# Kernel optimization log

Measured on AMD Instinct MI355X. Metric: run time of the kernel, lower is better.

Reference implementation:

```python
import jax, jax.numpy as jnp
import numpy as np

C = 1.0          # ball curvature (k = -1/c with c=1.0 in the torch module)
SQC = 1.0        # sqrt(C)
LN_EPS = 1e-5

def _artanh(x):
    return jnp.arctanh(jnp.clip(x, -1.0 + 1e-7, 1.0 - 1e-7))

def _norm(x):
    # last-dim L2 norm, clamped away from zero for stable division
    return jnp.clip(jnp.sqrt(jnp.sum(x * x, axis=-1, keepdims=True)), 1e-7, None)

def expmap0(u):
    un = _norm(u)
    return jnp.tanh(SQC * un) * u / (SQC * un)

def logmap0(y):
    yn = _norm(y)
    return _artanh(SQC * yn) * y / (SQC * yn)

def mobius_add(x, y):
    x2 = jnp.sum(x * x, axis=-1, keepdims=True)
    y2 = jnp.sum(y * y, axis=-1, keepdims=True)
    xy = jnp.sum(x * y, axis=-1, keepdims=True)
    num = (1.0 + 2.0 * C * xy + C * y2) * x + (1.0 - C * x2) * y
    den = 1.0 + 2.0 * C * xy + C * C * x2 * y2
    return num / jnp.clip(den, 1e-15, None)

def mobius_matvec(W, x):
    # W: [H, D], x: [B, D] -> [B, H]
    mx = x @ W.T
    xn = _norm(x)
    mxn = _norm(mx)
    res = jnp.tanh(mxn / xn * _artanh(SQC * xn)) * mx / (SQC * mxn)
    return jnp.where(mxn <= 1e-7, jnp.zeros_like(res), res)

def mobius_pointwise_mul(w, x):
    wx = w * x
    xn = _norm(x)
    wxn = _norm(wx)
    res = jnp.tanh(wxn / xn * _artanh(SQC * xn)) * wx / (SQC * wxn)
    return jnp.where(wxn <= 1e-7, jnp.zeros_like(res), res)

def layer_norm(x, g, b):
    mu = jnp.mean(x, axis=-1, keepdims=True)
    var = jnp.mean((x - mu) ** 2, axis=-1, keepdims=True)
    return (x - mu) * jax.lax.rsqrt(var + LN_EPS) * g + b

def one_rnn_transform(W, h, U, x, b):
    Wh = mobius_matvec(W, h)
    Ux = mobius_matvec(U, x)
    return mobius_add(mobius_add(Wh, Ux), b)

def setup_inputs() -> dict:
    key = jax.random.key(0)
    B, I, H = 65536, 256, 256
    k1, k2, k3, k4, k5 = jax.random.split(key, 5)
    stdv = 1.0 / np.sqrt(H)
    # points on the Poincare ball via expmap0 of small tangent vectors
    x = expmap0(0.02 * jax.random.normal(k1, (B, I), dtype=jnp.float32))
    hx = expmap0(0.02 * jax.random.normal(k2, (B, H), dtype=jnp.float32))
    weight_ih = jax.random.uniform(k3, (3 * H, I), dtype=jnp.float32, minval=-stdv, maxval=stdv)
    weight_hh = jax.random.uniform(k4, (3 * H, H), dtype=jnp.float32, minval=-stdv, maxval=stdv)
    bias = 0.01 * jax.random.normal(k5, (3, H), dtype=jnp.float32)
    ln_gamma = jnp.ones((3, H), dtype=jnp.float32)
    ln_beta = jnp.zeros((3, H), dtype=jnp.float32)
    return {"input": x, "hx": hx, "weight_ih": weight_ih, "weight_hh": weight_hh,
            "bias": bias, "ln_gamma": ln_gamma, "ln_beta": ln_beta}

def reference(input, hx, weight_ih, weight_hh, bias, ln_gamma, ln_beta):
    H = hx.shape[-1]
    W_ir, W_ih_, W_iz = weight_ih[:H], weight_ih[H:2*H], weight_ih[2*H:]
    W_hr, W_hh_, W_hz = weight_hh[:H], weight_hh[H:2*H], weight_hh[2*H:]
    b_r, b_h, b_z = bias[0], bias[1], bias[2]
    temp_z = logmap0(one_rnn_transform(W_hz, hx, W_iz, input, b_z))
    temp_r = logmap0(one_rnn_transform(W_hr, hx, W_ir, input, b_r))
    z_t = jax.nn.sigmoid(layer_norm(temp_z, ln_gamma[0], ln_beta[0]))
    r_t = jax.nn.sigmoid(layer_norm(temp_r, ln_gamma[1], ln_beta[1]))
    rh_t = mobius_pointwise_mul(r_t, hx)
    h_tilde = one_rnn_transform(W_hh_, rh_t, W_ih_, input, b_h)
    h_tilde = expmap0(jnp.tanh(layer_norm(logmap0(h_tilde), ln_gamma[2], ln_beta[2])))
    temp_1 = mobius_pointwise_mul(1.0 - z_t, hx)
    temp_2 = mobius_pointwise_mul(z_t, h_tilde)
    return mobius_add(temp_1, temp_2)
```

## Files before the change

### kernel.cpp

```cpp
#include <hip/hip_runtime.h>
#include <math.h>

#define HD  256
#define BM  16
#define NTH 256

typedef __attribute__((ext_vector_type(8))) short bf16x8;
typedef __attribute__((ext_vector_type(4))) float f32x4;

__device__ __forceinline__ float rcp_f(float x){ return __builtin_amdgcn_rcpf(x); }
__device__ __forceinline__ float tanh_f(float x){
  float ax = fabsf(x);
  float e  = __expf(-2.f*ax);
  float t  = (1.f - e) * rcp_f(1.f + e);
  return copysignf(t, x);
}
__device__ __forceinline__ float artanh_f(float v){
  v = fminf(fmaxf(v, -1.f + 1e-7f), 1.f - 1e-7f);
  return 0.5f * __logf((1.f + v) * rcp_f(1.f - v));
}
__device__ __forceinline__ float sigmoid_f(float v){ return rcp_f(1.f + __expf(-v)); }
__device__ __forceinline__ unsigned short f2bf(float f){
  unsigned u = __float_as_uint(f);
  u += 0x7FFFu + ((u >> 16) & 1u);
  return (unsigned short)(u >> 16);
}
__device__ __forceinline__ float bf2f(unsigned short h){
  return __uint_as_float(((unsigned)h) << 16);
}
__device__ __forceinline__ int swz(int R, int C){
  return R*HD + (((C >> 3) ^ (R & 7)) << 3) + (C & 7);
}

__global__ void convert_w_kernel(const float* __restrict__ Wih,
                                 const float* __restrict__ Whh,
                                 unsigned short* __restrict__ wb){
  int c = blockIdx.x * blockDim.x + threadIdx.x;
  if (c >= 6 * 8192) return;
  int mat = c >> 13;
  int ci  = c & 8191;
  int l = ci & 63, st = ci >> 6;
  int s = st & 7, ct = st >> 3;
  int col = ct * 16 + (l & 15);
  int k0  = s * 32 + (l >> 4) * 8;
  const float* src = (mat < 3) ? (Wih + (size_t)mat * HD * HD)
                               : (Whh + (size_t)(mat - 3) * HD * HD);
  const float* p = src + (size_t)col * HD + k0;
  unsigned short tmp[8];
  #pragma unroll
  for (int j = 0; j < 8; ++j) tmp[j] = f2bf(p[j]);
  *(bf16x8*)(wb + (size_t)mat * 65536 + (size_t)ci * 8) = *(bf16x8*)tmp;
}

__device__ __forceinline__ void gate_gemm(
    const unsigned short* ldsH, const unsigned short* __restrict__ wH,
    const unsigned short* ldsX, const unsigned short* __restrict__ wX,
    f32x4 A[4], f32x4 Bx[4], int wc, int lr, int lg, int l){
  #pragma unroll
  for (int n = 0; n < 4; ++n){
    A[n]  = (f32x4){0.f,0.f,0.f,0.f};
    Bx[n] = (f32x4){0.f,0.f,0.f,0.f};
  }
  #pragma unroll
  for (int s = 0; s < 8; ++s){
    int idx = lr*HD + (((4*s + lg) ^ (lr & 7)) << 3);
    bf16x8 ah = *(const bf16x8*)&ldsH[idx];
    bf16x8 ax = *(const bf16x8*)&ldsX[idx];
    #pragma unroll
    for (int n = 0; n < 4; ++n){
      int ct = wc*4 + n;
      int off = ((ct*8 + s)*64 + l)*8;
      bf16x8 bh = *(const bf16x8*)(wH + off);
      bf16x8 bx = *(const bf16x8*)(wX + off);
      A[n]  = __builtin_amdgcn_mfma_f32_16x16x32_bf16(ah, bh, A[n], 0, 0, 0);
      Bx[n] = __builtin_amdgcn_mfma_f32_16x16x32_bf16(ax, bx, Bx[n], 0, 0, 0);
    }
  }
}

__device__ __forceinline__ void gate_reduce_chain(
    const f32x4 (&A)[4], const f32x4 (&Bx)[4], const float (&bt)[4],
    float (*RED)[33], float (*kco)[9], float (*srow)[BM], const float* sbb,
    int rowA, int gidx, int t, int wc, int lr, int lg){
  float p[7][4];
  #pragma unroll
  for (int q = 0; q < 4; ++q){
    float a2=0.f,b2=0.f,ab=0.f,sA=0.f,sB=0.f,Ab=0.f,Bb=0.f;
    #pragma unroll
    for (int n = 0; n < 4; ++n){
      float ae = A[n][q], be = Bx[n][q], bv = bt[n];
      a2 = fmaf(ae,ae,a2); b2 = fmaf(be,be,b2); ab = fmaf(ae,be,ab);
      sA += ae; sB += be; Ab = fmaf(ae,bv,Ab); Bb = fmaf(be,bv,Bb);
    }
    p[0][q]=a2; p[1][q]=b2; p[2][q]=ab; p[3][q]=sA; p[4][q]=sB; p[5][q]=Ab; p[6][q]=Bb;
  }
  #pragma unroll
  for (int j = 0; j < 7; ++j)
    #pragma unroll
    for (int q = 0; q < 4; ++q){
      float v = p[j][q];
      v += __shfl_xor(v,1); v += __shfl_xor(v,2);
      v += __shfl_xor(v,4); v += __shfl_xor(v,8);
      p[j][q] = v;
    }
  if (lr == 0){
    #pragma unroll
    for (int q = 0; q < 4; ++q){
      int R = lg*4 + q;
      #pragma unroll
      for (int j = 0; j < 7; ++j) RED[R][wc*8 + j] = p[j][q];
    }
  }
  __syncthreads();
  if (t < BM){
    int R = t;
    float s[7];
    #pragma unroll
    for (int j = 0; j < 7; ++j)
      s[j] = RED[R][j] + RED[R][8+j] + RED[R][16+j] + RED[R][24+j];
    float bb  = sbb[gidx];
    float sbs = sbb[4+gidx];
    float an = srow[rowA][R], aa = srow[rowA+1][R];
    float bn = srow[0][R],    ba = srow[1][R];
    float mraw = sqrtf(s[0]); float mA = fmaxf(mraw, 1e-7f);
    float tA = tanh_f(mA / an * aa);
    float sa  = (mraw <= 1e-7f) ? 0.f : tA / mA;
    float x2a = (mraw <= 1e-7f) ? 0.f : tA*tA;
    float nraw = sqrtf(s[1]); float mB = fmaxf(nraw, 1e-7f);
    float tB = tanh_f(mB / bn * ba);
    float sb_ = (nraw <= 1e-7f) ? 0.f : tB / mB;
    float x2b = (nraw <= 1e-7f) ? 0.f : tB*tB;
    float xy = sa*sb_*s[2];
    float ca = 1.f + 2.f*xy + x2b;
    float cb = 1.f - x2a;
    float den = fmaxf(1.f + 2.f*xy + x2a*x2b, 1e-15f);
    float u = ca*sa/den, v = cb*sb_/den;
    float P2 = u*u*s[0] + 2.f*u*v*s[2] + v*v*s[1];
    float Pb = u*s[5] + v*s[6];
    float sP = u*s[3] + v*s[4];
    float ca2 = 1.f + 2.f*Pb + bb;
    float cb2 = 1.f - P2;
    float den2 = fmaxf(1.f + 2.f*Pb + P2*bb, 1e-15f);
    float pp = ca2/den2, ww = cb2/den2;
    float Q2 = pp*pp*P2 + 2.f*pp*ww*Pb + ww*ww*bb;
    float sQsum = pp*sP + ww*sbs;
    float qn = fmaxf(sqrtf(Q2), 1e-7f);
    float sQ = artanh_f(qn) / qn;
    float mu = sQ*sQsum*(1.f/HD);
    float e2 = sQ*sQ*Q2*(1.f/HD);
    float is = rsqrtf(e2 - mu*mu + 1e-5f);
    kco[R][0] = sQ*pp*u;  kco[R][1] = sQ*pp*v;  kco[R][2] = sQ*ww;
    kco[R][3] = mu;       kco[R][4] = is;
  }
  __syncthreads();
}

__global__ __launch_bounds__(NTH, 2) void mobius_gru_mfma(
    const float* __restrict__ x, const float* __restrict__ hx,
    const unsigned short* __restrict__ wbih, const unsigned short* __restrict__ wbhh,
    const float* __restrict__ bias, const float* __restrict__ gam,
    const float* __restrict__ bet, float* __restrict__ out, int B){
  __shared__ unsigned short xb[BM*HD];
  __shared__ unsigned short hb[BM*HD];
  __shared__ float RED[BM][33];
  __shared__ float kco[BM][9];
  __shared__ float srow[8][BM];
  __shared__ float sbb[8];

  const int t  = threadIdx.x;
  const int l  = t & 63;
  const int lr = l & 15, lg = l >> 4;
  const int wc = t >> 6;
  const size_t row0 = (size_t)blockIdx.x * BM;

  {
    float* spart = &RED[0][0];
    int r = t >> 4, seg = t & 15;
    const float* xp = x  + (row0 + r)*HD + seg*16;
    const float* hp = hx + (row0 + r)*HD + seg*16;
    float sx = 0.f, sh = 0.f;
    #pragma unroll
    for (int i = 0; i < 4; ++i){
      int c = seg*16 + i*4;
      int di = swz(r, c);
      float4 v = *(const float4*)(xp + i*4);
      sx += v.x*v.x + v.y*v.y + v.z*v.z + v.w*v.w;
      ushort4 o = { f2bf(v.x), f2bf(v.y), f2bf(v.z), f2bf(v.w) };
      *(ushort4*)&xb[di] = o;
      v = *(const float4*)(hp + i*4);
      sh += v.x*v.x + v.y*v.y + v.z*v.z + v.w*v.w;
      ushort4 o2 = { f2bf(v.x), f2bf(v.y), f2bf(v.z), f2bf(v.w) };
      *(ushort4*)&hb[di] = o2;
    }
    spart[r*16 + seg] = sx; spart[256 + r*16 + seg] = sh;
  }
  if (t >= 64 && t < 256){
    int g = (t >> 6) - 1;
    float4 b4 = *(const float4*)&bias[g*HD + (t & 63)*4];
    float p2 = b4.x*b4.x + b4.y*b4.y + b4.z*b4.z + b4.w*b4.w;
    float ps = b4.x + b4.y + b4.z + b4.w;
    #pragma unroll
    for (int m = 1; m <= 32; m <<= 1){ p2 += __shfl_xor(p2, m); ps += __shfl_xor(ps, m); }
    if ((t & 63) == 0){ sbb[g] = p2; sbb[4+g] = ps; }
  }
  __syncthreads();
  if (t < BM){
    float* spart = &RED[0][0];
    float sx = 0.f, sh = 0.f;
    #pragma unroll
    for (int i = 0; i < 16; ++i){ sx += spart[t*16 + i]; sh += spart[256 + t*16 + i]; }
    float xn = fmaxf(sqrtf(sx), 1e-7f);
    float hn = fmaxf(sqrtf(sh), 1e-7f);
    srow[0][t] = xn; srow[1][t] = artanh_f(xn);
    srow[2][t] = hn; srow[3][t] = artanh_f(hn);
  }
  __syncthreads();

  f32x4 A[4], Bx[4];
  float bt[4], gv[4], bv[4];
  unsigned ztp[4][2];
  float hvreg[4][4];

  #pragma unroll
  for (int n = 0; n < 4; ++n){
    int C = wc*64 + n*16 + lr;
    bt[n] = bias[2*HD + C]; gv[n] = gam[C]; bv[n] = bet[C];
  }
  gate_gemm(hb, wbhh + 2*65536, xb, wbih + 2*65536, A, Bx, wc, lr, lg, l);
  gate_reduce_chain(A, Bx, bt, RED, kco, srow, sbb, 2, 2, t, wc, lr, lg);
  #pragma unroll
  for (int q = 0; q < 4; ++q){
    int R = lg*4 + q;
    float KA=kco[R][0], KB=kco[R][1], Kb=kco[R][2], mu=kco[R][3], is=kco[R][4];
    #pragma unroll
    for (int n = 0; n < 4; ++n){
      float ln = (KA*A[n][q] + KB*Bx[n][q] + Kb*bt[n] - mu)*is*gv[n] + bv[n];
      unsigned zb = f2bf(sigmoid_f(ln));
      if ((q & 1) == 0) ztp[n][q>>1] = zb;
      else              ztp[n][q>>1] |= (zb << 16);
    }
  }

  #pragma unroll
  for (int n = 0; n < 4; ++n){
    int C = wc*64 + n*16 + lr;
    bt[n] = bias[C]; gv[n] = gam[HD + C]; bv[n] = bet[HD + C];
  }
  gate_gemm(hb, wbhh, xb, wbih, A, Bx, wc, lr, lg, l);
  gate_reduce_chain(A, Bx, bt, RED, kco, srow, sbb, 2, 0, t, wc, lr, lg);
  {
    #pragma unroll
    for (int q = 0; q < 4; ++q){
      int R = lg*4 + q;
      float KA=kco[R][0], KB=kco[R][1], Kb=kco[R][2], mu=kco[R][3], is=kco[R][4];
      float acc = 0.f;
      #pragma unroll
      for (int n = 0; n < 4; ++n){
        int C = wc*64 + n*16 + lr;
        float hv = bf2f(hb[swz(R, C)]);
        hvreg[n][q] = hv;
        float ln = (KA*A[n][q] + KB*Bx[n][q] + Kb*bt[n] - mu)*is*gv[n] + bv[n];
        float rhv = sigmoid_f(ln) * hv;
        Bx[n][q] = rhv;
        acc = fmaf(rhv, rhv, acc);
      }
      float v2 = acc;
      v2 += __shfl_xor(v2,1); v2 += __shfl_xor(v2,2);
      v2 += __shfl_xor(v2,4); v2 += __shfl_xor(v2,8);
      if (lr == 0) RED[R][wc*8] = v2;
    }
  }
  __syncthreads();
  if (t < BM){
    int R = t;
    float s0 = RED[R][0] + RED[R][8] + RED[R][16] + RED[R][24];
    float wraw = sqrtf(s0); float wn = fmaxf(wraw, 1e-7f);
    float s = tanh_f(wn / srow[2][R] * srow[3][R]);
    float sc = (wraw <= 1e-7f) ? 0.f : s / wn;
    float rn = fmaxf((wraw <= 1e-7f) ? 0.f : fabsf(s), 1e-7f);
    kco[R][0] = sc; srow[4][R] = rn; srow[5][R] = artanh_f(rn);
  }
  __syncthreads();
  #pragma unroll
  for (int q = 0; q < 4; ++q){
    int R = lg*4 + q;
    float sc = kco[R][0];
    #pragma unroll
    for (int n = 0; n < 4; ++n){
      int C = wc*64 + n*16 + lr;
      hb[swz(R, C)] = f2bf(sc * Bx[n][q]);
    }
  }
  __syncthreads();

  #pragma unroll
  for (int n = 0; n < 4; ++n){
    int C = wc*64 + n*16 + lr;
    bt[n] = bias[HD + C]; gv[n] = gam[2*HD + C]; bv[n] = bet[2*HD + C];
  }
  gate_gemm(hb, wbhh + 65536, xb, wbih + 65536, A, Bx, wc, lr, lg, l);
  gate_reduce_chain(A, Bx, bt, RED, kco, srow, sbb, 4, 1, t, wc, lr, lg);
  {
    #pragma unroll
    for (int q = 0; q < 4; ++q){
      int R = lg*4 + q;
      float KA=kco[R][0], KB=kco[R][1], Kb=kco[R][2], mu=kco[R][3], is=kco[R][4];
      float acc = 0.f;
      #pragma unroll
      for (int n = 0; n < 4; ++n){
        float ln = (KA*A[n][q] + KB*Bx[n][q] + Kb*bt[n] - mu)*is*gv[n] + bv[n];
        float uv = tanh_f(ln);
        A[n][q] = uv;
        acc = fmaf(uv, uv, acc);
      }
      float v2 = acc;
      v2 += __shfl_xor(v2,1); v2 += __shfl_xor(v2,2);
      v2 += __shfl_xor(v2,4); v2 += __shfl_xor(v2,8);
      if (lr == 0) RED[R][wc*8] = v2;
    }
  }
  __syncthreads();
  if (t < BM){
    int R = t;
    float s0 = RED[R][0] + RED[R][8] + RED[R][16] + RED[R][24];
    float unraw = sqrtf(s0);
    float un = fmaxf(unraw, 1e-7f);
    float es = tanh_f(un) / un;
    float htn = fmaxf(es * unraw, 1e-7f);
    kco[R][0] = es; srow[6][R] = htn; srow[7][R] = artanh_f(htn);
  }
  __syncthreads();

  #pragma unroll
  for (int q = 0; q < 4; ++q){
    int R = lg*4 + q;
    float es = kco[R][0];
    float a1 = 0.f, a2 = 0.f, a12 = 0.f;
    #pragma unroll
    for (int n = 0; n < 4; ++n){
      unsigned zp = ztp[n][q >> 1];
      float zv = __uint_as_float((q & 1) ? (zp & 0xFFFF0000u) : (zp << 16));
      float w2v = zv * es * A[n][q];
      float w1v = (1.f - zv) * hvreg[n][q];
      A[n][q]  = w1v;
      Bx[n][q] = w2v;
      a1 = fmaf(w1v, w1v, a1); a2 = fmaf(w2v, w2v, a2); a12 = fmaf(w1v, w2v, a12);
    }
    float v1 = a1, v2 = a2, v3 = a12;
    v1 += __shfl_xor(v1,1); v2 += __shfl_xor(v2,1); v3 += __shfl_xor(v3,1);
    v1 += __shfl_xor(v1,2); v2 += __shfl_xor(v2,2); v3 += __shfl_xor(v3,2);
    v1 += __shfl_xor(v1,4); v2 += __shfl_xor(v2,4); v3 += __shfl_xor(v3,4);
    v1 += __shfl_xor(v1,8); v2 += __shfl_xor(v2,8); v3 += __shfl_xor(v3,8);
    if (lr == 0){
      RED[R][wc*8]   = v1;
      RED[R][wc*8+1] = v2;
      RED[R][wc*8+2] = v3;
    }
  }
  __syncthreads();
  if (t < BM){
    int R = t;
    float s1  = RED[R][0] + RED[R][8]  + RED[R][16] + RED[R][24];
    float s2  = RED[R][1] + RED[R][9]  + RED[R][17] + RED[R][25];
    float s12 = RED[R][2] + RED[R][10] + RED[R][18] + RED[R][26];
    float raw1 = sqrtf(s1); float n1 = fmaxf(raw1, 1e-7f);
    float ss1 = tanh_f(n1 / srow[2][R] * srow[3][R]);
    float sc1 = (raw1 <= 1e-7f) ? 0.f : ss1 / n1;
    float t1  = (raw1 <= 1e-7f) ? 0.f : ss1*ss1;
    float raw2 = sqrtf(s2); float n2 = fmaxf(raw2, 1e-7f);
    float ss2 = tanh_f(n2 / srow[6][R] * srow[7][R]);
    float sc2 = (raw2 <= 1e-7f) ? 0.f : ss2 / n2;
    float t2  = (raw2 <= 1e-7f) ? 0.f : ss2*ss2;
    float xy = sc1*sc2*s12;
    float ca = 1.f + 2.f*xy + t2;
    float cb = 1.f - t1;
    float den = fmaxf(1.f + 2.f*xy + t1*t2, 1e-15f);
    kco[R][0] = ca*sc1/den;
    kco[R][1] = cb*sc2/den;
  }
  __syncthreads();
  #pragma unroll
  for (int q = 0; q < 4; ++q){
    int R = lg*4 + q;
    float cw1 = kco[R][0], cw2 = kco[R][1];
    #pragma unroll
    for (int n = 0; n < 4; ++n){
      int C = wc*64 + n*16 + lr;
      out[(row0 + R)*HD + C] = cw1*A[n][q] + cw2*Bx[n][q];
    }
  }
}

extern "C" void kernel_launch(void* const* d_in, const int* in_sizes, int n_in,
                              void* d_out, int out_size, void* d_ws, size_t ws_size,
                              hipStream_t stream){
  const float* x    = (const float*)d_in[0];
  const float* hx   = (const float*)d_in[1];
  const float* Wih  = (const float*)d_in[2];
  const float* Whh  = (const float*)d_in[3];
  const float* bias = (const float*)d_in[4];
  const float* gam  = (const float*)d_in[5];
  const float* bet  = (const float*)d_in[6];
  float* out = (float*)d_out;
  unsigned short* wb = (unsigned short*)d_ws;
  const int B = in_sizes[0] / HD;

  hipLaunchKernelGGL(convert_w_kernel, dim3(192), dim3(256), 0, stream, Wih, Whh, wb);
  hipLaunchKernelGGL(mobius_gru_mfma, dim3(B / BM), dim3(NTH), 0, stream,
                     x, hx, wb, wb + 3*65536, bias, gam, bet, out, B);
}
```

Baseline: 222.8 us.

## Run each 16-row tile on a single wave, using shuffles instead of block barriers

The block shrinks from four waves to one. Each wave now computes all 256 output columns for its 16 rows, keeping 16 MFMA tiles per operand in registers. The shared-memory reductions and __syncthreads rounds are replaced with cross-lane shuffles, and gate order becomes r, h, z. The r*h scaling is applied to the GEMM output rather than the LDS input, and z's inputs are re-read from LDS at the end. The aim is to remove barrier and LDS-reduction overhead, at the cost of much higher register pressure from 32 f32x4 accumulators and each wave streaming the full weight set.

Result: slower. 532.6 us (+139.1%).

```diff
diff --git a/kernel.cpp b/kernel.cpp
--- a/kernel.cpp
+++ b/kernel.cpp
@@ -3,7 +3,7 @@
 
 #define HD  256
 #define BM  16
-#define NTH 256
+#define NTH 64
 
 typedef __attribute__((ext_vector_type(8))) short bf16x8;
 typedef __attribute__((ext_vector_type(4))) float f32x4;
@@ -52,47 +52,52 @@
   *(bf16x8*)(wb + (size_t)mat * 65536 + (size_t)ci * 8) = *(bf16x8*)tmp;
 }
 
-__device__ __forceinline__ void gate_gemm(
-    const unsigned short* ldsH, const unsigned short* __restrict__ wH,
-    const unsigned short* ldsX, const unsigned short* __restrict__ wX,
-    f32x4 A[4], f32x4 Bx[4], int wc, int lr, int lg, int l){
-  #pragma unroll
-  for (int n = 0; n < 4; ++n){
+__device__ __forceinline__ void gemm16(
+    const unsigned short* ldsA, const unsigned short* __restrict__ wA,
+    const unsigned short* ldsB, const unsigned short* __restrict__ wB,
+    f32x4* A, f32x4* Bx, int lr, int lg, int l){
+  #pragma unroll
+  for (int n = 0; n < 16; ++n){
     A[n]  = (f32x4){0.f,0.f,0.f,0.f};
     Bx[n] = (f32x4){0.f,0.f,0.f,0.f};
   }
-  #pragma unroll
+  #pragma unroll 2
   for (int s = 0; s < 8; ++s){
     int idx = lr*HD + (((4*s + lg) ^ (lr & 7)) << 3);
-    bf16x8 ah = *(const bf16x8*)&ldsH[idx];
-    bf16x8 ax = *(const bf16x8*)&ldsX[idx];
-    #pragma unroll
-    for (int n = 0; n < 4; ++n){
-      int ct = wc*4 + n;
-      int off = ((ct*8 + s)*64 + l)*8;
-      bf16x8 bh = *(const bf16x8*)(wH + off);
-      bf16x8 bx = *(const bf16x8*)(wX + off);
-      A[n]  = __builtin_amdgcn_mfma_f32_16x16x32_bf16(ah, bh, A[n], 0, 0, 0);
-      Bx[n] = __builtin_amdgcn_mfma_f32_16x16x32_bf16(ax, bx, Bx[n], 0, 0, 0);
-    }
-  }
-}
-
-__device__ __forceinline__ void gate_reduce_chain(
-    const f32x4 (&A)[4], const f32x4 (&Bx)[4], const float (&bt)[4],
-    float (*RED)[33], float (*kco)[9], float (*srow)[BM], const float* sbb,
-    int rowA, int gidx, int t, int wc, int lr, int lg){
+    bf16x8 fa = *(const bf16x8*)&ldsA[idx];
+    bf16x8 fb = *(const bf16x8*)&ldsB[idx];
+    #pragma unroll
+    for (int n = 0; n < 16; ++n){
+      int off = ((n*8 + s)*64 + l)*8;
+      bf16x8 wa = *(const bf16x8*)(wA + off);
+      bf16x8 wb_ = *(const bf16x8*)(wB + off);
+      A[n]  = __builtin_amdgcn_mfma_f32_16x16x32_bf16(fa, wa, A[n], 0, 0, 0);
+      Bx[n] = __builtin_amdgcn_mfma_f32_16x16x32_bf16(fb, wb_, Bx[n], 0, 0, 0);
+    }
+  }
+}
+
+__device__ __forceinline__ void reduce7w(
+    const f32x4* A, const f32x4* Bx, const float* __restrict__ bgate,
+    int lr, int l, float* s7){
   float p[7][4];
   #pragma unroll
-  for (int q = 0; q < 4; ++q){
-    float a2=0.f,b2=0.f,ab=0.f,sA=0.f,sB=0.f,Ab=0.f,Bb=0.f;
-    #pragma unroll
-    for (int n = 0; n < 4; ++n){
-      float ae = A[n][q], be = Bx[n][q], bv = bt[n];
-      a2 = fmaf(ae,ae,a2); b2 = fmaf(be,be,b2); ab = fmaf(ae,be,ab);
-      sA += ae; sB += be; Ab = fmaf(ae,bv,Ab); Bb = fmaf(be,bv,Bb);
-    }
-    p[0][q]=a2; p[1][q]=b2; p[2][q]=ab; p[3][q]=sA; p[4][q]=sB; p[5][q]=Ab; p[6][q]=Bb;
+  for (int j = 0; j < 7; ++j)
+    #pragma unroll
+    for (int q = 0; q < 4; ++q) p[j][q] = 0.f;
+  #pragma unroll
+  for (int n = 0; n < 16; ++n){
+    float btv = bgate[n*16 + lr];
+    #pragma unroll
+    for (int q = 0; q < 4; ++q){
+      float ae = A[n][q], be = Bx[n][q];
+      p[0][q] = fmaf(ae,ae,p[0][q]);
+      p[1][q] = fmaf(be,be,p[1][q]);
+      p[2][q] = fmaf(ae,be,p[2][q]);
+      p[3][q] += ae; p[4][q] += be;
+      p[5][q] = fmaf(ae,btv,p[5][q]);
+      p[6][q] = fmaf(be,btv,p[6][q]);
+    }
   }
   #pragma unroll
   for (int j = 0; j < 7; ++j)
@@ -103,56 +108,49 @@
       v += __shfl_xor(v,4); v += __shfl_xor(v,8);
       p[j][q] = v;
     }
-  if (lr == 0){
-    #pragma unroll
-    for (int q = 0; q < 4; ++q){
-      int R = lg*4 + q;
-      #pragma unroll
-      for (int j = 0; j < 7; ++j) RED[R][wc*8 + j] = p[j][q];
-    }
-  }
-  __syncthreads();
-  if (t < BM){
-    int R = t;
-    float s[7];
-    #pragma unroll
-    for (int j = 0; j < 7; ++j)
-      s[j] = RED[R][j] + RED[R][8+j] + RED[R][16+j] + RED[R][24+j];
-    float bb  = sbb[gidx];
-    float sbs = sbb[4+gidx];
-    float an = srow[rowA][R], aa = srow[rowA+1][R];
-    float bn = srow[0][R],    ba = srow[1][R];
-    float mraw = sqrtf(s[0]); float mA = fmaxf(mraw, 1e-7f);
-    float tA = tanh_f(mA / an * aa);
-    float sa  = (mraw <= 1e-7f) ? 0.f : tA / mA;
-    float x2a = (mraw <= 1e-7f) ? 0.f : tA*tA;
-    float nraw = sqrtf(s[1]); float mB = fmaxf(nraw, 1e-7f);
-    float tB = tanh_f(mB / bn * ba);
-    float sb_ = (nraw <= 1e-7f) ? 0.f : tB / mB;
-    float x2b = (nraw <= 1e-7f) ? 0.f : tB*tB;
-    float xy = sa*sb_*s[2];
-    float ca = 1.f + 2.f*xy + x2b;
-    float cb = 1.f - x2a;
-    float den = fmaxf(1.f + 2.f*xy + x2a*x2b, 1e-15f);
-    float u = ca*sa/den, v = cb*sb_/den;
-    float P2 = u*u*s[0] + 2.f*u*v*s[2] + v*v*s[1];
-    float Pb = u*s[5] + v*s[6];
-    float sP = u*s[3] + v*s[4];
-    float ca2 = 1.f + 2.f*Pb + bb;
-    float cb2 = 1.f - P2;
-    float den2 = fmaxf(1.f + 2.f*Pb + P2*bb, 1e-15f);
-    float pp = ca2/den2, ww = cb2/den2;
-    float Q2 = pp*pp*P2 + 2.f*pp*ww*Pb + ww*ww*bb;
-    float sQsum = pp*sP + ww*sbs;
-    float qn = fmaxf(sqrtf(Q2), 1e-7f);
-    float sQ = artanh_f(qn) / qn;
-    float mu = sQ*sQsum*(1.f/HD);
-    float e2 = sQ*sQ*Q2*(1.f/HD);
-    float is = rsqrtf(e2 - mu*mu + 1e-5f);
-    kco[R][0] = sQ*pp*u;  kco[R][1] = sQ*pp*v;  kco[R][2] = sQ*ww;
-    kco[R][3] = mu;       kco[R][4] = is;
-  }
-  __syncthreads();
+  int row = l & 15, src = (row >> 2) << 4, qq = row & 3;
+  #pragma unroll
+  for (int j = 0; j < 7; ++j){
+    float t0 = __shfl(p[j][0], src);
+    float t1 = __shfl(p[j][1], src);
+    float t2 = __shfl(p[j][2], src);
+    float t3 = __shfl(p[j][3], src);
+    s7[j] = (qq == 0) ? t0 : (qq == 1) ? t1 : (qq == 2) ? t2 : t3;
+  }
+}
+
+__device__ __forceinline__ void chain5(
+    const float* s, float bb, float sbs,
+    float an, float aa, float bn, float ba, float* o){
+  float mraw = sqrtf(s[0]); float mA = fmaxf(mraw, 1e-7f);
+  float tA = tanh_f(mA / an * aa);
+  float sa  = (mraw <= 1e-7f) ? 0.f : tA / mA;
+  float x2a = (mraw <= 1e-7f) ? 0.f : tA*tA;
+  float nraw = sqrtf(s[1]); float mB = fmaxf(nraw, 1e-7f);
+  float tB = tanh_f(mB / bn * ba);
+  float sb_ = (nraw <= 1e-7f) ? 0.f : tB / mB;
+  float x2b = (nraw <= 1e-7f) ? 0.f : tB*tB;
+  float xy = sa*sb_*s[2];
+  float ca = 1.f + 2.f*xy + x2b;
+  float cb = 1.f - x2a;
+  float den = fmaxf(1.f + 2.f*xy + x2a*x2b, 1e-15f);
+  float u = ca*sa/den, v = cb*sb_/den;
+  float P2 = u*u*s[0] + 2.f*u*v*s[2] + v*v*s[1];
+  float Pb = u*s[5] + v*s[6];
+  float sP = u*s[3] + v*s[4];
+  float ca2 = 1.f + 2.f*Pb + bb;
+  float cb2 = 1.f - P2;
+  float den2 = fmaxf(1.f + 2.f*Pb + P2*bb, 1e-15f);
+  float pp = ca2/den2, ww = cb2/den2;
+  float Q2 = pp*pp*P2 + 2.f*pp*ww*Pb + ww*ww*bb;
+  float sQsum = pp*sP + ww*sbs;
+  float qn = fmaxf(sqrtf(Q2), 1e-7f);
+  float sQ = artanh_f(qn) / qn;
+  float mu = sQ*sQsum*(1.f/HD);
+  float e2 = sQ*sQ*Q2*(1.f/HD);
+  float is = rsqrtf(e2 - mu*mu + 1e-5f);
+  o[0] = sQ*pp*u;  o[1] = sQ*pp*v;  o[2] = sQ*ww;
+  o[3] = mu;       o[4] = is;
 }
 
 __global__ __launch_bounds__(NTH, 2) void mobius_gru_mfma(
@@ -162,231 +160,233 @@
     const float* __restrict__ bet, float* __restrict__ out, int B){
   __shared__ unsigned short xb[BM*HD];
   __shared__ unsigned short hb[BM*HD];
-  __shared__ float RED[BM][33];
-  __shared__ float kco[BM][9];
-  __shared__ float srow[8][BM];
-  __shared__ float sbb[8];
-
-  const int t  = threadIdx.x;
-  const int l  = t & 63;
+  __shared__ unsigned short rub[BM*HD];
+
+  const int l  = threadIdx.x;
   const int lr = l & 15, lg = l >> 4;
-  const int wc = t >> 6;
+  const int myrow = l & 15;
   const size_t row0 = (size_t)blockIdx.x * BM;
 
-  {
-    float* spart = &RED[0][0];
-    int r = t >> 4, seg = t & 15;
-    const float* xp = x  + (row0 + r)*HD + seg*16;
-    const float* hp = hx + (row0 + r)*HD + seg*16;
-    float sx = 0.f, sh = 0.f;
-    #pragma unroll
-    for (int i = 0; i < 4; ++i){
-      int c = seg*16 + i*4;
+  float sx = 0.f, sh = 0.f;
+  {
+    int r = l >> 2, seg = l & 3;
+    const float* xp = x  + (row0 + r)*HD;
+    const float* hp = hx + (row0 + r)*HD;
+    #pragma unroll
+    for (int i = 0; i < 16; ++i){
+      int c = i*16 + seg*4;
       int di = swz(r, c);
-      float4 v = *(const float4*)(xp + i*4);
+      float4 v = *(const float4*)(xp + c);
       sx += v.x*v.x + v.y*v.y + v.z*v.z + v.w*v.w;
       ushort4 o = { f2bf(v.x), f2bf(v.y), f2bf(v.z), f2bf(v.w) };
       *(ushort4*)&xb[di] = o;
-      v = *(const float4*)(hp + i*4);
-      sh += v.x*v.x + v.y*v.y + v.z*v.z + v.w*v.w;
-      ushort4 o2 = { f2bf(v.x), f2bf(v.y), f2bf(v.z), f2bf(v.w) };
+      float4 w = *(const float4*)(hp + c);
+      sh += w.x*w.x + w.y*w.y + w.z*w.z + w.w*w.w;
+      ushort4 o2 = { f2bf(w.x), f2bf(w.y), f2bf(w.z), f2bf(w.w) };
       *(ushort4*)&hb[di] = o2;
     }
-    spart[r*16 + seg] = sx; spart[256 + r*16 + seg] = sh;
-  }
-  if (t >= 64 && t < 256){
-    int g = (t >> 6) - 1;
-    float4 b4 = *(const float4*)&bias[g*HD + (t & 63)*4];
+  }
+  sx += __shfl_xor(sx,1); sx += __shfl_xor(sx,2);
+  sh += __shfl_xor(sh,1); sh += __shfl_xor(sh,2);
+  float xn, xa, hn, ha;
+  {
+    float sxr = __shfl(sx, myrow << 2);
+    float shr = __shfl(sh, myrow << 2);
+    xn = fmaxf(sqrtf(sxr), 1e-7f); xa = artanh_f(xn);
+    hn = fmaxf(sqrtf(shr), 1e-7f); ha = artanh_f(hn);
+  }
+  float bbv[3], sbv[3];
+  #pragma unroll
+  for (int g = 0; g < 3; ++g){
+    float4 b4 = *(const float4*)&bias[g*HD + l*4];
     float p2 = b4.x*b4.x + b4.y*b4.y + b4.z*b4.z + b4.w*b4.w;
     float ps = b4.x + b4.y + b4.z + b4.w;
     #pragma unroll
-    for (int m = 1; m <= 32; m <<= 1){ p2 += __shfl_xor(p2, m); ps += __shfl_xor(ps, m); }
-    if ((t & 63) == 0){ sbb[g] = p2; sbb[4+g] = ps; }
-  }
-  __syncthreads();
-  if (t < BM){
-    float* spart = &RED[0][0];
-    float sx = 0.f, sh = 0.f;
-    #pragma unroll
-    for (int i = 0; i < 16; ++i){ sx += spart[t*16 + i]; sh += spart[256 + t*16 + i]; }
-    float xn = fmaxf(sqrtf(sx), 1e-7f);
-    float hn = fmaxf(sqrtf(sh), 1e-7f);
-    srow[0][t] = xn; srow[1][t] = artanh_f(xn);
-    srow[2][t] = hn; srow[3][t] = artanh_f(hn);
-  }
-  __syncthreads();
-
-  f32x4 A[4], Bx[4];
-  float bt[4], gv[4], bv[4];
-  unsigned ztp[4][2];
-  float hvreg[4][4];
-
-  #pragma unroll
-  for (int n = 0; n < 4; ++n){
-    int C = wc*64 + n*16 + lr;
-    bt[n] = bias[2*HD + C]; gv[n] = gam[C]; bv[n] = bet[C];
-  }
-  gate_gemm(hb, wbhh + 2*65536, xb, wbih + 2*65536, A, Bx, wc, lr, lg, l);
-  gate_reduce_chain(A, Bx, bt, RED, kco, srow, sbb, 2, 2, t, wc, lr, lg);
+    for (int m = 1; m <= 32; m <<= 1){ p2 += __shfl_xor(p2,m); ps += __shfl_xor(ps,m); }
+    bbv[g] = p2; sbv[g] = ps;
+  }
+
+  f32x4 A[16], Bx2[16];
+  float s7[7], o5[5];
+
+  gemm16(hb, wbhh, xb, wbih, A, Bx2, lr, lg, l);
+  reduce7w(A, Bx2, bias, lr, l, s7);
+  chain5(s7, bbv[0], sbv[0], hn, ha, xn, xa, o5);
+  float scr, rn, ra;
+  {
+    float KA[4],KB[4],Kb[4],MU[4],IS[4], rh2q[4];
+    #pragma unroll
+    for (int q = 0; q < 4; ++q){
+      int R = lg*4 + q;
+      KA[q]=__shfl(o5[0],R); KB[q]=__shfl(o5[1],R); Kb[q]=__shfl(o5[2],R);
+      MU[q]=__shfl(o5[3],R); IS[q]=__shfl(o5[4],R);
+      rh2q[q] = 0.f;
+    }
+    #pragma unroll
+    for (int n = 0; n < 16; ++n){
+      int C = n*16 + lr;
+      float btv = bias[C];
+      float gv  = gam[HD + C];
+      float bv  = bet[HD + C];
+      #pragma unroll
+      for (int q = 0; q < 4; ++q){
+        int R = lg*4 + q;
+        float hv = bf2f(hb[swz(R, C)]);
+        float ln = (KA[q]*A[n][q] + KB[q]*Bx2[n][q] + Kb[q]*btv - MU[q])*IS[q]*gv + bv;
+        float rhv = sigmoid_f(ln) * hv;
+        rub[swz(R, C)] = f2bf(rhv);
+        rh2q[q] = fmaf(rhv, rhv, rh2q[q]);
+      }
+    }
+    #pragma unroll
+    for (int q = 0; q < 4; ++q){
+      float v = rh2q[q];
+      v += __shfl_xor(v,1); v += __shfl_xor(v,2);
+      v += __shfl_xor(v,4); v += __shfl_xor(v,8);
+      rh2q[q] = v;
+    }
+    int src = (myrow >> 2) << 4, qq = myrow & 3;
+    float t0=__shfl(rh2q[0],src), t1=__shfl(rh2q[1],src);
+    float t2=__shfl(rh2q[2],src), t3=__shfl(rh2q[3],src);
+    float s0 = (qq==0)?t0:(qq==1)?t1:(qq==2)?t2:t3;
+    float wraw = sqrtf(s0); float wn = fmaxf(wraw, 1e-7f);
+    float sv = tanh_f(wn / hn * ha);
+    scr = (wraw <= 1e-7f) ? 0.f : sv / wn;
+    rn  = fmaxf((wraw <= 1e-7f) ? 0.f : fabsf(sv), 1e-7f);
+    ra  = artanh_f(rn);
+  }
+
+  gemm16(rub, wbhh + 65536, xb, wbih + 65536, A, Bx2, lr, lg, l);
+  {
+    float scq[4];
+    #pragma unroll
+    for (int q = 0; q < 4; ++q) scq[q] = __shfl(scr, lg*4 + q);
+    #pragma unroll
+    for (int n = 0; n < 16; ++n)
+      #pragma unroll
+      for (int q = 0; q < 4; ++q) A[n][q] *= scq[q];
+  }
+  reduce7w(A, Bx2, bias + HD, lr, l, s7);
+  chain5(s7, bbv[1], sbv[1], rn, ra, xn, xa, o5);
+  float es, htn, hta;
+  {
+    float KA[4],KB[4],Kb[4],MU[4],IS[4], u2q[4];
+    #pragma unroll
+    for (int q = 0; q < 4; ++q){
+      int R = lg*4 + q;
+      KA[q]=__shfl(o5[0],R); KB[q]=__shfl(o5[1],R); Kb[q]=__shfl(o5[2],R);
+      MU[q]=__shfl(o5[3],R); IS[q]=__shfl(o5[4],R);
+      u2q[q] = 0.f;
+    }
+    #pragma unroll
+    for (int n = 0; n < 16; ++n){
+      int C = n*16 + lr;
+      float btv = bias[HD + C];
+      float gv  = gam[2*HD + C];
+      float bv  = bet[2*HD + C];
+      #pragma unroll
+      for (int q = 0; q < 4; ++q){
+        int R = lg*4 + q;
+        float ln = (KA[q]*A[n][q] + KB[q]*Bx2[n][q] + Kb[q]*btv - MU[q])*IS[q]*gv + bv;
+        float uv = tanh_f(ln);
+        rub[swz(R, C)] = f2bf(uv);
+        u2q[q] = fmaf(uv, uv, u2q[q]);
+      }
+    }
+    #pragma unroll
+    for (int q = 0; q < 4; ++q){
+      float v = u2q[q];
+      v += __shfl_xor(v,1); v += __shfl_xor(v,2);
+      v += __shfl_xor(v,4); v += __shfl_xor(v,8);
+      u2q[q] = v;
+    }
+    int src = (myrow >> 2) << 4, qq = myrow & 3;
+    float t0=__shfl(u2q[0],src), t1=__shfl(u2q[1],src);
+    float t2=__shfl(u2q[2],src), t3=__shfl(u2q[3],src);
+    float s0 = (qq==0)?t0:(qq==1)?t1:(qq==2)?t2:t3;
+    float unraw = sqrtf(s0);
+    float un = fmaxf(unraw, 1e-7f);
+    es  = tanh_f(un) / un;
+    htn = fmaxf(es * unraw, 1e-7f);
+    hta = artanh_f(htn);
+  }
+
+  gemm16(hb, wbhh + 2*65536, xb, wbih + 2*65536, A, Bx2, lr, lg, l);
+  reduce7w(A, Bx2, bias + 2*HD, lr, l, s7);
+  chain5(s7, bbv[2], sbv[2], hn, ha, xn, xa, o5);
+  float cw1, cw2;
+  {
+    float KA[4],KB[4],Kb[4],MU[4],IS[4],ESQ[4], a1q[4], a2q[4], a12q[4];
+    #pragma unroll
+    for (int q = 0; q < 4; ++q){
+      int R = lg*4 + q;
+      KA[q]=__shfl(o5[0],R); KB[q]=__shfl(o5[1],R); Kb[q]=__shfl(o5[2],R);
+      MU[q]=__shfl(o5[3],R); IS[q]=__shfl(o5[4],R);
+      ESQ[q]=__shfl(es, R);
+      a1q[q]=a2q[q]=a12q[q]=0.f;
+    }
+    #pragma unroll
+    for (int n = 0; n < 16; ++n){
+      int C = n*16 + lr;
+      float btv = bias[2*HD + C];
+      float gv  = gam[C];
+      float bv  = bet[C];
+      #pragma unroll
+      for (int q = 0; q < 4; ++q){
+        int R = lg*4 + q;
+        float ln = (KA[q]*A[n][q] + KB[q]*Bx2[n][q] + Kb[q]*btv - MU[q])*IS[q]*gv + bv;
+        float zv = sigmoid_f(ln);
+        float uv = bf2f(rub[swz(R, C)]);
+        float hv = bf2f(hb[swz(R, C)]);
+        float w2 = zv * ESQ[q] * uv;
+        float w1 = (1.f - zv) * hv;
+        A[n][q]  = w1;
+        Bx2[n][q] = w2;
+        a1q[q]  = fmaf(w1,w1,a1q[q]);
+        a2q[q]  = fmaf(w2,w2,a2q[q]);
+        a12q[q] = fmaf(w1,w2,a12q[q]);
+      }
+    }
+    #pragma unroll
+    for (int q = 0; q < 4; ++q){
+      float v1 = a1q[q], v2 = a2q[q], v3 = a12q[q];
+      v1 += __shfl_xor(v1,1); v2 += __shfl_xor(v2,1); v3 += __shfl_xor(v3,1);
+      v1 += __shfl_xor(v1,2); v2 += __shfl_xor(v2,2); v3 += __shfl_xor(v3,2);
+      v1 += __shfl_xor(v1,4); v2 += __shfl_xor(v2,4); v3 += __shfl_xor(v3,4);
+      v1 += __shfl_xor(v1,8); v2 += __shfl_xor(v2,8); v3 += __shfl_xor(v3,8);
+      a1q[q]=v1; a2q[q]=v2; a12q[q]=v3;
+    }
+    int src = (myrow >> 2) << 4, qq = myrow & 3;
+    float t0,t1,t2,t3, s1,s2,s12;
+    t0=__shfl(a1q[0],src); t1=__shfl(a1q[1],src); t2=__shfl(a1q[2],src); t3=__shfl(a1q[3],src);
+    s1 = (qq==0)?t0:(qq==1)?t1:(qq==2)?t2:t3;
+    t0=__shfl(a2q[0],src); t1=__shfl(a2q[1],src); t2=__shfl(a2q[2],src); t3=__shfl(a2q[3],src);
+    s2 = (qq==0)?t0:(qq==1)?t1:(qq==2)?t2:t3;
+    t0=__shfl(a12q[0],src); t1=__shfl(a12q[1],src); t2=__shfl(a12q[2],src); t3=__shfl(a12q[3],src);
+    s12 = (qq==0)?t0:(qq==1)?t1:(qq==2)?t2:t3;
+    float raw1 = sqrtf(s1); float n1 = fmaxf(raw1, 1e-7f);
+    float ss1 = tanh_f(n1 / hn * ha);
+    float sc1 = (raw1 <= 1e-7f) ? 0.f : ss1 / n1;
+    float tt1 = (raw1 <= 1e-7f) ? 0.f : ss1*ss1;
+    float raw2 = sqrtf(s2); float n2 = fmaxf(raw2, 1e-7f);
+    float ss2 = tanh_f(n2 / htn * hta);
+    float sc2 = (raw2 <= 1e-7f) ? 0.f : ss2 / n2;
+    float tt2 = (raw2 <= 1e-7f) ? 0.f : ss2*ss2;
+    float xy = sc1*sc2*s12;
+    float ca = 1.f + 2.f*xy + tt2;
+    float cb = 1.f - tt1;
+    float den = fmaxf(1.f + 2.f*xy + tt1*tt2, 1e-15f);
+    cw1 = ca*sc1/den;
+    cw2 = cb*sc2/den;
+  }
   #pragma unroll
   for (int q = 0; q < 4; ++q){
     int R = lg*4 + q;
-    float KA=kco[R][0], KB=kco[R][1], Kb=kco[R][2], mu=kco[R][3], is=kco[R][4];
-    #pragma unroll
-    for (int n = 0; n < 4; ++n){
-      float ln = (KA*A[n][q] + KB*Bx[n][q] + Kb*bt[n] - mu)*is*gv[n] + bv[n];
-      unsigned zb = f2bf(sigmoid_f(ln));
-      if ((q & 1) == 0) ztp[n][q>>1] = zb;
-      else              ztp[n][q>>1] |= (zb << 16);
-    }
-  }
-
-  #pragma unroll
-  for (int n = 0; n < 4; ++n){
-    int C = wc*64 + n*16 + lr;
-    bt[n] = bias[C]; gv[n] = gam[HD + C]; bv[n] = bet[HD + C];
-  }
-  gate_gemm(hb, wbhh, xb, wbih, A, Bx, wc, lr, lg, l);
-  gate_reduce_chain(A, Bx, bt, RED, kco, srow, sbb, 2, 0, t, wc, lr, lg);
-  {
-    #pragma unroll
-    for (int q = 0; q < 4; ++q){
-      int R = lg*4 + q;
-      float KA=kco[R][0], KB=kco[R][1], Kb=kco[R][2], mu=kco[R][3], is=kco[R][4];
-      float acc = 0.f;
-      #pragma unroll
-      for (int n = 0; n < 4; ++n){
-        int C = wc*64 + n*16 + lr;
-        float hv = bf2f(hb[swz(R, C)]);
-        hvreg[n][q] = hv;
-        float ln = (KA*A[n][q] + KB*Bx[n][q] + Kb*bt[n] - mu)*is*gv[n] + bv[n];
-        float rhv = sigmoid_f(ln) * hv;
-        Bx[n][q] = rhv;
-        acc = fmaf(rhv, rhv, acc);
-      }
-      float v2 = acc;
-      v2 += __shfl_xor(v2,1); v2 += __shfl_xor(v2,2);
-      v2 += __shfl_xor(v2,4); v2 += __shfl_xor(v2,8);
-      if (lr == 0) RED[R][wc*8] = v2;
-    }
-  }
-  __syncthreads();
-  if (t < BM){
-    int R = t;
-    float s0 = RED[R][0] + RED[R][8] + RED[R][16] + RED[R][24];
-    float wraw = sqrtf(s0); float wn = fmaxf(wraw, 1e-7f);
-    float s = tanh_f(wn / srow[2][R] * srow[3][R]);
-    float sc = (wraw <= 1e-7f) ? 0.f : s / wn;
-    float rn = fmaxf((wraw <= 1e-7f) ? 0.f : fabsf(s), 1e-7f);
-    kco[R][0] = sc; srow[4][R] = rn; srow[5][R] = artanh_f(rn);
-  }
-  __syncthreads();
-  #pragma unroll
-  for (int q = 0; q < 4; ++q){
-    int R = lg*4 + q;
-    float sc = kco[R][0];
-    #pragma unroll
-    for (int n = 0; n < 4; ++n){
-      int C = wc*64 + n*16 + lr;
-      hb[swz(R, C)] = f2bf(sc * Bx[n][q]);
-    }
-  }
-  __syncthreads();
-
-  #pragma unroll
-  for (int n = 0; n < 4; ++n){
-    int C = wc*64 + n*16 + lr;
-    bt[n] = bias[HD + C]; gv[n] = gam[2*HD + C]; bv[n] = bet[2*HD + C];
-  }
-  gate_gemm(hb, wbhh + 65536, xb, wbih + 65536, A, Bx, wc, lr, lg, l);
-  gate_reduce_chain(A, Bx, bt, RED, kco, srow, sbb, 4, 1, t, wc, lr, lg);
-  {
-    #pragma unroll
-    for (int q = 0; q < 4; ++q){
-      int R = lg*4 + q;
-      float KA=kco[R][0], KB=kco[R][1], Kb=kco[R][2], mu=kco[R][3], is=kco[R][4];
-      float acc = 0.f;
-      #pragma unroll
-      for (int n = 0; n < 4; ++n){
-        float ln = (KA*A[n][q] + KB*Bx[n][q] + Kb*bt[n] - mu)*is*gv[n] + bv[n];
-        float uv = tanh_f(ln);
-        A[n][q] = uv;
-        acc = fmaf(uv, uv, acc);
-      }
-      float v2 = acc;
-      v2 += __shfl_xor(v2,1); v2 += __shfl_xor(v2,2);
-      v2 += __shfl_xor(v2,4); v2 += __shfl_xor(v2,8);
-      if (lr == 0) RED[R][wc*8] = v2;
-    }
-  }
-  __syncthreads();
-  if (t < BM){
-    int R = t;
-    float s0 = RED[R][0] + RED[R][8] + RED[R][16] + RED[R][24];
-    float unraw = sqrtf(s0);
-    float un = fmaxf(unraw, 1e-7f);
-    float es = tanh_f(un) / un;
-    float htn = fmaxf(es * unraw, 1e-7f);
-    kco[R][0] = es; srow[6][R] = htn; srow[7][R] = artanh_f(htn);
-  }
-  __syncthreads();
-
-  #pragma unroll
-  for (int q = 0; q < 4; ++q){
-    int R = lg*4 + q;
-    float es = kco[R][0];
-    float a1 = 0.f, a2 = 0.f, a12 = 0.f;
-    #pragma unroll
-    for (int n = 0; n < 4; ++n){
-      unsigned zp = ztp[n][q >> 1];
-      float zv = __uint_as_float((q & 1) ? (zp & 0xFFFF0000u) : (zp << 16));
-      float w2v = zv * es * A[n][q];
-      float w1v = (1.f - zv) * hvreg[n][q];
-      A[n][q]  = w1v;
-      Bx[n][q] = w2v;
-      a1 = fmaf(w1v, w1v, a1); a2 = fmaf(w2v, w2v, a2); a12 = fmaf(w1v, w2v, a12);
-    }
-    float v1 = a1, v2 = a2, v3 = a12;
-    v1 += __shfl_xor(v1,1); v2 += __shfl_xor(v2,1); v3 += __shfl_xor(v3,1);
-    v1 += __shfl_xor(v1,2); v2 += __shfl_xor(v2,2); v3 += __shfl_xor(v3,2);
-    v1 += __shfl_xor(v1,4); v2 += __shfl_xor(v2,4); v3 += __shfl_xor(v3,4);
-    v1 += __shfl_xor(v1,8); v2 += __shfl_xor(v2,8); v3 += __shfl_xor(v3,8);
-    if (lr == 0){
-      RED[R][wc*8]   = v1;
-      RED[R][wc*8+1] = v2;
-      RED[R][wc*8+2] = v3;
-    }
-  }
-  __syncthreads();
-  if (t < BM){
-    int R = t;
-    float s1  = RED[R][0] + RED[R][8]  + RED[R][16] + RED[R][24];
-    float s2  = RED[R][1] + RED[R][9]  + RED[R][17] + RED[R][25];
-    float s12 = RED[R][2] + RED[R][10] + RED[R][18] + RED[R][26];
-    float raw1 = sqrtf(s1); float n1 = fmaxf(raw1, 1e-7f);
-    float ss1 = tanh_f(n1 / srow[2][R] * srow[3][R]);
-    float sc1 = (raw1 <= 1e-7f) ? 0.f : ss1 / n1;
-    float t1  = (raw1 <= 1e-7f) ? 0.f : ss1*ss1;
-    float raw2 = sqrtf(s2); float n2 = fmaxf(raw2, 1e-7f);
-    float ss2 = tanh_f(n2 / srow[6][R] * srow[7][R]);
-    float sc2 = (raw2 <= 1e-7f) ? 0.f : ss2 / n2;
-    float t2  = (raw2 <= 1e-7f) ? 0.f : ss2*ss2;
-    float xy = sc1*sc2*s12;
-    float ca = 1.f + 2.f*xy + t2;
-    float cb = 1.f - t1;
-    float den = fmaxf(1.f + 2.f*xy + t1*t2, 1e-15f);
-    kco[R][0] = ca*sc1/den;
-    kco[R][1] = cb*sc2/den;
-  }
-  __syncthreads();
-  #pragma unroll
-  for (int q = 0; q < 4; ++q){
-    int R = lg*4 + q;
-    float cw1 = kco[R][0], cw2 = kco[R][1];
-    #pragma unroll
-    for (int n = 0; n < 4; ++n){
-      int C = wc*64 + n*16 + lr;
-      out[(row0 + R)*HD + C] = cw1*A[n][q] + cw2*Bx[n][q];
+    float c1 = __shfl(cw1, R), c2 = __shfl(cw2, R);
+    #pragma unroll
+    for (int n = 0; n < 16; ++n){
+      int C = n*16 + lr;
+      out[(row0 + R)*HD + C] = c1*A[n][q] + c2*Bx2[n][q];
     }
   }
 }
```
